# Performance work log

Measured on AMD Instinct MI355X. Metric: run time of the kernel, lower is better.

The kernel has to match this reference:

```python
import jax, jax.numpy as jnp
import numpy as np

HIDDEN = 128
N_NODES = 50000
N_EDGES = 640000


def setup_inputs() -> dict:
    key = jax.random.key(0)
    k1, k2, k3, k4, k5, k6, k7 = jax.random.split(key, 7)
    z = jax.random.normal(k1, (N_NODES, HIDDEN), dtype=jnp.float32)
    edge_index = jax.random.randint(k2, (2, N_EDGES), 0, N_NODES, dtype=jnp.int64)
    # Linear params (torch default uniform(-1/sqrt(fan_in), 1/sqrt(fan_in)))
    b1 = 1.0 / np.sqrt(2 * HIDDEN)
    W1 = jax.random.uniform(k3, (HIDDEN, 2 * HIDDEN), jnp.float32, -b1, b1)
    bias1 = jax.random.uniform(k4, (HIDDEN,), jnp.float32, -b1, b1)
    b2 = 1.0 / np.sqrt(HIDDEN)
    W2 = jax.random.uniform(k5, (1, HIDDEN), jnp.float32, -b2, b2)
    bias2 = jax.random.uniform(k6, (1,), jnp.float32, -b2, b2)
    return {"z": z, "W1": W1, "bias1": bias1, "W2": W2, "bias2": bias2,
            "edge_index": edge_index}


def reference(z, W1, bias1, W2, bias2, edge_index):
    # Gather endpoint embeddings: [E, H] each
    z_src = z[edge_index[0]]
    z_dst = z[edge_index[1]]
    h = jnp.concatenate([z_src, z_dst], axis=-1)  # [E, 2H]
    h = jax.nn.relu(h @ W1.T + bias1)             # [E, H]
    out = h @ W2.T + bias2                        # [E, 1]
    return out.reshape(-1)
```

## Files before the change

kernel.cpp:

```cpp
#include <hip/hip_runtime.h>
#include <hip/hip_bf16.h>


#define N_NODES 50000
#define N_EDGES 640000
#define H 128

using bf16 = __hip_bfloat16;
typedef __attribute__((ext_vector_type(8))) short short8;
typedef __attribute__((ext_vector_type(4))) float f32x4;

#define GLD_LDS16(g, l)                                                     \
  __builtin_amdgcn_global_load_lds(                                         \
      (const __attribute__((address_space(1))) void*)(g),                   \
      (__attribute__((address_space(3))) void*)(l), 16, 0, 0)

static __device__ __forceinline__ short bfbits(float x) {
  __hip_bfloat16 h = __float2bfloat16(x);
  return *reinterpret_cast<short*>(&h);
}

static __device__ __forceinline__ short8 pack8(float4 a, float4 b) {
  short8 r;
  r[0] = bfbits(a.x); r[1] = bfbits(a.y); r[2] = bfbits(a.z); r[3] = bfbits(a.w);
  r[4] = bfbits(b.x); r[5] = bfbits(b.y); r[6] = bfbits(b.z); r[7] = bfbits(b.w);
  return r;
}

__global__ __launch_bounds__(256) void w_to_bf16(const float* __restrict__ W1,
                                                 bf16* __restrict__ Wb) {
  const int u = blockIdx.x * 256 + threadIdx.x;
  const int o = u >> 4, k8 = (u & 15) * 8;
  const float4* src = reinterpret_cast<const float4*>(
      W1 + (size_t)(o & (H - 1)) * (2 * H) + (o >> 7) * H + k8);
  *reinterpret_cast<short8*>(Wb + (size_t)o * H + k8) = pack8(src[0], src[1]);
}

#define HP 136

__global__ __launch_bounds__(256) void precompute_uv(
    const float* __restrict__ z, const bf16* __restrict__ Wb,
    const float* __restrict__ bias1, bf16* __restrict__ U,
    bf16* __restrict__ V) {
  __shared__ float ldsF[32 * H];
  __shared__ bf16 ldsH[32 * HP];
  const int tid = threadIdx.x;
  const int lane = tid & 63;
  const int s = tid >> 6;
  const int l15 = lane & 15, quad = lane >> 4;
  const int nodebase = blockIdx.x * 32;

  {
    int r0 = nodebase + s * 8;
    if (r0 > N_NODES - 8) r0 = N_NODES - 8;
    const float* gsrc = z + (size_t)r0 * H + lane * 4;
    float* ldst = ldsF + s * 8 * H;
#pragma unroll
    for (int j = 0; j < 4; ++j) GLD_LDS16(gsrc + j * 256, ldst + j * 256);
  }

  short8 wf[4][4];
#pragma unroll
  for (int t = 0; t < 4; ++t) {
    const bf16* wp = Wb + (size_t)(s * 64 + t * 16 + l15) * H + quad * 8;
#pragma unroll
    for (int q = 0; q < 4; ++q)
      wf[t][q] = *reinterpret_cast<const short8*>(wp + q * 32);
  }

  __syncthreads();

  {
    const int row = tid >> 3, off = (tid & 7) * 16;
    const float4* fp = reinterpret_cast<const float4*>(ldsF + row * H + off);
    const float4 a = fp[0], b = fp[1], c = fp[2], d = fp[3];
    *reinterpret_cast<short8*>(&ldsH[row * HP + off]) = pack8(a, b);
    *reinterpret_cast<short8*>(&ldsH[row * HP + off + 8]) = pack8(c, d);
  }
  __syncthreads();

  short8 zf[2][4];
#pragma unroll
  for (int m = 0; m < 2; ++m)
#pragma unroll
    for (int q = 0; q < 4; ++q)
      zf[m][q] = *reinterpret_cast<const short8*>(
          &ldsH[(m * 16 + l15) * HP + quad * 8 + q * 32]);

  f32x4 acc[2][4] = {};
#pragma unroll
  for (int m = 0; m < 2; ++m)
#pragma unroll
    for (int t = 0; t < 4; ++t)
#pragma unroll
      for (int q = 0; q < 4; ++q)
        acc[m][t] =
            __builtin_amdgcn_mfma_f32_16x16x32_bf16(wf[t][q], zf[m][q], acc[m][t], 0, 0, 0);

  bf16* epi = reinterpret_cast<bf16*>(ldsF);
#pragma unroll
  for (int m = 0; m < 2; ++m) {
    const int nl = m * 16 + l15;
#pragma unroll
    for (int t = 0; t < 4; ++t) {
      const int o = s * 64 + t * 16 + quad * 4;
      const float4 bv = *reinterpret_cast<const float4*>(bias1 + (o & (H - 1)));
      ushort4 st;
      st.x = (unsigned short)bfbits(acc[m][t][0] + 0.5f * bv.x);
      st.y = (unsigned short)bfbits(acc[m][t][1] + 0.5f * bv.y);
      st.z = (unsigned short)bfbits(acc[m][t][2] + 0.5f * bv.z);
      st.w = (unsigned short)bfbits(acc[m][t][3] + 0.5f * bv.w);
      *reinterpret_cast<ushort4*>(epi + nl * 256 + o) = st;
    }
  }
  __syncthreads();

#pragma unroll
  for (int half = 0; half < 2; ++half) {
    bf16* base = half ? V : U;
#pragma unroll
    for (int it = 0; it < 2; ++it) {
      const int nl = s * 8 + it * 4 + (lane >> 4);
      const int oc = (lane & 15) * 8;
      const short8 v = *reinterpret_cast<const short8*>(epi + nl * 256 + half * H + oc);
      const int n = nodebase + nl;
      if (n < N_NODES)
        *reinterpret_cast<short8*>(base + (size_t)n * H + oc) = v;
    }
  }
}

static __device__ __forceinline__ void acc2(unsigned u, unsigned v,
                                            float w2lo, float w2hi, float& sum) {
  const float ulo = __uint_as_float(u << 16);
  const float uhi = __uint_as_float(u & 0xffff0000u);
  const float vlo = __uint_as_float(v << 16);
  const float vhi = __uint_as_float(v & 0xffff0000u);
  float h0 = fmaxf(ulo + vlo, 0.f);
  float h1 = fmaxf(uhi + vhi, 0.f);
  sum = fmaf(h0, w2lo, sum);
  sum = fmaf(h1, w2hi, sum);
}

__global__ __launch_bounds__(256, 4) void edge_decode(
    const int* __restrict__ eidx, const bf16* __restrict__ Ub,
    const bf16* __restrict__ Vb, const float* __restrict__ W2,
    const float* __restrict__ bias2, float* __restrict__ out) {
  const int lane = threadIdx.x & 63;
  const int e8 = lane & 7;
  const int w = blockIdx.x * 4 + (int)(threadIdx.x >> 6);
  const int chunk = w * 64;

  float w2r[16];
  const float4* wp = reinterpret_cast<const float4*>(W2 + e8 * 16);
#pragma unroll
  for (int q = 0; q < 4; ++q) {
    const float4 wv = wp[q];
    w2r[q * 4 + 0] = wv.x; w2r[q * 4 + 1] = wv.y;
    w2r[q * 4 + 2] = wv.z; w2r[q * 4 + 3] = wv.w;
  }
  const float b2 = bias2[0];

  const int src = eidx[chunk + lane];
  const int dst = eidx[N_EDGES + chunk + lane];
  const uint4* U4 = reinterpret_cast<const uint4*>(Ub);
  const uint4* V4 = reinterpret_cast<const uint4*>(Vb);

  float res = 0.f;
#pragma unroll
  for (int half = 0; half < 2; ++half) {
    uint4 ua[4], ub[4], va[4], vb[4];
#pragma unroll
    for (int j = 0; j < 4; ++j) {
      const int i = half * 4 + j;
      const int sl = (lane & 56) | i;
      const int s_i = __shfl(src, sl);
      const int d_i = __shfl(dst, sl);
      const uint4* up = U4 + (size_t)s_i * 16 + e8 * 2;
      const uint4* vp = V4 + (size_t)d_i * 16 + e8 * 2;
      ua[j] = up[0]; ub[j] = up[1];
      va[j] = vp[0]; vb[j] = vp[1];
    }
    asm volatile("" ::
        "v"(ua[0].x), "v"(ua[1].x), "v"(ua[2].x), "v"(ua[3].x),
        "v"(ub[0].x), "v"(ub[1].x), "v"(ub[2].x), "v"(ub[3].x),
        "v"(va[0].x), "v"(va[1].x), "v"(va[2].x), "v"(va[3].x),
        "v"(vb[0].x), "v"(vb[1].x), "v"(vb[2].x), "v"(vb[3].x));
    __builtin_amdgcn_sched_barrier(0);
#pragma unroll
    for (int j = 0; j < 4; ++j) {
      const int i = half * 4 + j;
      float sum = 0.f;
      acc2(ua[j].x, va[j].x, w2r[0],  w2r[1],  sum);
      acc2(ua[j].y, va[j].y, w2r[2],  w2r[3],  sum);
      acc2(ua[j].z, va[j].z, w2r[4],  w2r[5],  sum);
      acc2(ua[j].w, va[j].w, w2r[6],  w2r[7],  sum);
      acc2(ub[j].x, vb[j].x, w2r[8],  w2r[9],  sum);
      acc2(ub[j].y, vb[j].y, w2r[10], w2r[11], sum);
      acc2(ub[j].z, vb[j].z, w2r[12], w2r[13], sum);
      acc2(ub[j].w, vb[j].w, w2r[14], w2r[15], sum);
      sum += __shfl_xor(sum, 1);
      sum += __shfl_xor(sum, 2);
      sum += __shfl_xor(sum, 4);
      if (e8 == i) res = sum + b2;
    }
  }
  out[chunk + lane] = res;
}

extern "C" void kernel_launch(void* const* d_in, const int* in_sizes, int n_in,
                              void* d_out, int out_size, void* d_ws, size_t ws_size,
                              hipStream_t stream) {
  const float* z     = (const float*)d_in[0];
  const float* W1    = (const float*)d_in[1];
  const float* bias1 = (const float*)d_in[2];
  const float* W2    = (const float*)d_in[3];
  const float* bias2 = (const float*)d_in[4];
  const int*   eidx  = (const int*)d_in[5];
  float* out = (float*)d_out;

  bf16* U  = (bf16*)d_ws;
  bf16* V  = U + (size_t)N_NODES * H;
  bf16* Wb = V + (size_t)N_NODES * H;

  hipLaunchKernelGGL(w_to_bf16, dim3(16), dim3(256), 0, stream, W1, Wb);
  hipLaunchKernelGGL(precompute_uv, dim3((N_NODES + 31) / 32), dim3(256), 0,
                     stream, z, Wb, bias1, U, V);
  hipLaunchKernelGGL(edge_decode, dim3(N_EDGES / 64 / 4), dim3(256), 0, stream,
                     eidx, U, V, W2, bias2, out);
}
```

Baseline: 137.6 us.

## Counting-sort edges by source node to improve gather locality in decode

```diff
diff --git a/kernel.cpp b/kernel.cpp
--- a/kernel.cpp
+++ b/kernel.cpp
@@ -130,6 +130,46 @@
   }
 }
 
+
+__global__ __launch_bounds__(256) void src_hist(const int* __restrict__ eidx,
+                                                int* __restrict__ cnt) {
+  const int e = blockIdx.x * 256 + threadIdx.x;
+  atomicAdd(&cnt[eidx[e]], 1);
+}
+
+__global__ __launch_bounds__(256) void src_resv(const int* __restrict__ cnt,
+                                                int* __restrict__ cur,
+                                                int* __restrict__ total) {
+  __shared__ int sh[256];
+  __shared__ int sbase;
+  const int t = threadIdx.x;
+  const int n = blockIdx.x * 256 + t;
+  const int c = (n < N_NODES) ? cnt[n] : 0;
+  int incl = c;
+  sh[t] = incl;
+  for (int off = 1; off < 256; off <<= 1) {
+    __syncthreads();
+    const int add = (t >= off) ? sh[t - off] : 0;
+    __syncthreads();
+    incl += add;
+    sh[t] = incl;
+  }
+  __syncthreads();
+  if (t == 255) sbase = atomicAdd(total, incl);
+  __syncthreads();
+  if (n < N_NODES) cur[n] = sbase + incl - c;
+}
+
+__global__ __launch_bounds__(256) void src_scat(
+    const int* __restrict__ eidx, int* __restrict__ cur,
+    unsigned long long* __restrict__ sorted) {
+  const int e = blockIdx.x * 256 + threadIdx.x;
+  const unsigned s = (unsigned)eidx[e];
+  const unsigned d = (unsigned)eidx[N_EDGES + e];
+  const int pos = atomicAdd(&cur[s], 1);
+  sorted[pos] = ((unsigned long long)(unsigned)e << 32) | (d << 16) | s;
+}
+
 static __device__ __forceinline__ void acc2(unsigned u, unsigned v,
                                             float w2lo, float w2hi, float& sum) {
   const float ulo = __uint_as_float(u << 16);
@@ -143,7 +183,7 @@
 }
 
 __global__ __launch_bounds__(256, 4) void edge_decode(
-    const int* __restrict__ eidx, const bf16* __restrict__ Ub,
+    const unsigned long long* __restrict__ sorted, const bf16* __restrict__ Ub,
     const bf16* __restrict__ Vb, const float* __restrict__ W2,
     const float* __restrict__ bias2, float* __restrict__ out) {
   const int lane = threadIdx.x & 63;
@@ -161,8 +201,10 @@
   }
   const float b2 = bias2[0];
 
-  const int src = eidx[chunk + lane];
-  const int dst = eidx[N_EDGES + chunk + lane];
+  const unsigned long long ent = sorted[chunk + lane];
+  const int src = (int)(ent & 0xffffu);
+  const int dst = (int)((ent >> 16) & 0xffffu);
+  const int eid = (int)(ent >> 32);
   const uint4* U4 = reinterpret_cast<const uint4*>(Ub);
   const uint4* V4 = reinterpret_cast<const uint4*>(Vb);
 
@@ -181,12 +223,6 @@
       ua[j] = up[0]; ub[j] = up[1];
       va[j] = vp[0]; vb[j] = vp[1];
     }
-    asm volatile("" ::
-        "v"(ua[0].x), "v"(ua[1].x), "v"(ua[2].x), "v"(ua[3].x),
-        "v"(ub[0].x), "v"(ub[1].x), "v"(ub[2].x), "v"(ub[3].x),
-        "v"(va[0].x), "v"(va[1].x), "v"(va[2].x), "v"(va[3].x),
-        "v"(vb[0].x), "v"(vb[1].x), "v"(vb[2].x), "v"(vb[3].x));
-    __builtin_amdgcn_sched_barrier(0);
 #pragma unroll
     for (int j = 0; j < 4; ++j) {
       const int i = half * 4 + j;
@@ -205,7 +241,7 @@
       if (e8 == i) res = sum + b2;
     }
   }
-  out[chunk + lane] = res;
+  out[eid] = res;
 }
 
 extern "C" void kernel_launch(void* const* d_in, const int* in_sizes, int n_in,
@@ -222,10 +258,23 @@
   bf16* U  = (bf16*)d_ws;
   bf16* V  = U + (size_t)N_NODES * H;
   bf16* Wb = V + (size_t)N_NODES * H;
+  unsigned long long* sorted =
+      (unsigned long long*)(Wb + 256 * H);
+  int* cnt   = (int*)(sorted + N_EDGES);
+  int* total = cnt + N_NODES;
+  int* cur   = total + 16;
+
+  hipMemsetAsync(cnt, 0, (N_NODES + 16) * sizeof(int), stream);
 
   hipLaunchKernelGGL(w_to_bf16, dim3(16), dim3(256), 0, stream, W1, Wb);
+  hipLaunchKernelGGL(src_hist, dim3(N_EDGES / 256), dim3(256), 0, stream,
+                     eidx, cnt);
+  hipLaunchKernelGGL(src_resv, dim3((N_NODES + 255) / 256), dim3(256), 0,
+                     stream, cnt, cur, total);
+  hipLaunchKernelGGL(src_scat, dim3(N_EDGES / 256), dim3(256), 0, stream,
+                     eidx, cur, sorted);
   hipLaunchKernelGGL(precompute_uv, dim3((N_NODES + 31) / 32), dim3(256), 0,
                      stream, z, Wb, bias1, U, V);
   hipLaunchKernelGGL(edge_decode, dim3(N_EDGES / 64 / 4), dim3(256), 0, stream,
-                     eidx, U, V, W2, bias2, out);
-}
+                     sorted, U, V, W2, bias2, out);
+}
```

After: 210.6 us. 53.1% more time.
